# Kernel tuning notes

Measured on AMD Instinct MI355X. Metric: run time of the kernel, lower is better.

## Reference

```python
import jax, jax.numpy as jnp
import numpy as np

F = 1024      # features
CF = 768      # context_features
H = 8         # num_heads
D = 64        # head_features
MID = H * D   # 512
SCALE = D ** -0.5


def _ln(x, g, b):
    m = jnp.mean(x, axis=-1, keepdims=True)
    v = jnp.var(x, axis=-1, keepdims=True)
    return (x - m) / jnp.sqrt(v + 1e-5) * g + b


def _attention(x, ctx, ng, nb, ncg, ncb, wq, wkv, wo, bo):
    # pre-norms (Attention.forward)
    xn = _ln(x, ng, nb)
    cn = _ln(ctx, ncg, ncb)
    q = xn @ wq                              # [b, n, MID]
    k, v = jnp.split(cn @ wkv, 2, axis=-1)   # [b, m, MID] each
    b, n, _ = q.shape
    m = k.shape[1]
    q = q.reshape(b, n, H, D).transpose(0, 2, 1, 3)  # b h n d
    k = k.reshape(b, m, H, D).transpose(0, 2, 1, 3)
    v = v.reshape(b, m, H, D).transpose(0, 2, 1, 3)
    sim = jnp.einsum('bhnd,bhmd->bhnm', q, k) * SCALE   # use_rel_pos=False
    attn = jax.nn.softmax(sim, axis=-1)
    out = jnp.einsum('bhnm,bhmd->bhnd', attn, v)
    out = out.transpose(0, 2, 1, 3).reshape(b, n, MID)
    return out @ wo + bo


def setup_inputs() -> dict:
    key = jax.random.key(0)
    ks = jax.random.split(key, 16)
    s = 0.02
    inp = {
        'x': jax.random.normal(ks[0], (4, 2048, F), jnp.float32),
        'context': jax.random.normal(ks[1], (4, 512, CF), jnp.float32),
        # self-attention params
        'sa_ng': jnp.ones((F,), jnp.float32),
        'sa_nb': jnp.zeros((F,), jnp.float32),
        'sa_ncg': jnp.ones((F,), jnp.float32),
        'sa_ncb': jnp.zeros((F,), jnp.float32),
        'sa_wq': jax.random.normal(ks[2], (F, MID), jnp.float32) * s,
        'sa_wkv': jax.random.normal(ks[3], (F, 2 * MID), jnp.float32) * s,
        'sa_wo': jax.random.normal(ks[4], (MID, F), jnp.float32) * s,
        'sa_bo': jnp.zeros((F,), jnp.float32),
        # cross-attention params
        'ca_ng': jnp.ones((F,), jnp.float32),
        'ca_nb': jnp.zeros((F,), jnp.float32),
        'ca_ncg': jnp.ones((CF,), jnp.float32),
        'ca_ncb': jnp.zeros((CF,), jnp.float32),
        'ca_wq': jax.random.normal(ks[5], (F, MID), jnp.float32) * s,
        'ca_wkv': jax.random.normal(ks[6], (CF, 2 * MID), jnp.float32) * s,
        'ca_wo': jax.random.normal(ks[7], (MID, F), jnp.float32) * s,
        'ca_bo': jnp.zeros((F,), jnp.float32),
    }
    return inp


def reference(x, context,
              sa_ng, sa_nb, sa_ncg, sa_ncb, sa_wq, sa_wkv, sa_wo, sa_bo,
              ca_ng, ca_nb, ca_ncg, ca_ncb, ca_wq, ca_wkv, ca_wo, ca_bo):
    # AttentionBlock.forward: x = self_attn(x) + x; x = cross_attn(x, ctx) + x
    x = _attention(x, x, sa_ng, sa_nb, sa_ncg, sa_ncb, sa_wq, sa_wkv, sa_wo, sa_bo) + x
    x = _attention(x, context, ca_ng, ca_nb, ca_ncg, ca_ncb, ca_wq, ca_wkv, ca_wo, ca_bo) + x
    return x
```

## Files before the change

kernel.cpp:

```cpp
#include <hip/hip_runtime.h>
#include <hip/hip_bf16.h>

typedef __bf16 bf16x8 __attribute__((ext_vector_type(8)));
typedef float  f32x4  __attribute__((ext_vector_type(4)));

#define MFMA16(a, b, c) __builtin_amdgcn_mfma_f32_16x16x32_bf16((a), (b), (c), 0, 0, 0)

__device__ __forceinline__ float fast_exp2(float x) {
#if __has_builtin(__builtin_amdgcn_exp2f)
    return __builtin_amdgcn_exp2f(x);
#else
    return exp2f(x);
#endif
}

__device__ __forceinline__ void async16(void* lds, const void* g) {
    __builtin_amdgcn_global_load_lds(
        (const __attribute__((address_space(1))) unsigned int*)g,
        (__attribute__((address_space(3))) unsigned int*)lds, 16, 0, 0);
}

__device__ __forceinline__ void tconv_tile(const float* __restrict__ W,
                                           __bf16* __restrict__ WT,
                                           int K, int N, int id, int nbx,
                                           __bf16 (*t)[65]) {
    int n0 = (id % nbx) * 64, k0 = (id / nbx) * 64;
    int tx = threadIdx.x & 63, ty = threadIdx.x >> 6;
#pragma unroll
    for (int r = ty; r < 64; r += 4)
        t[r][tx] = (__bf16)W[(size_t)(k0 + r) * N + n0 + tx];
    __syncthreads();
#pragma unroll
    for (int rr = ty; rr < 64; rr += 4)
        WT[(size_t)(n0 + rr) * K + k0 + tx] = t[tx][rr];
}

__global__ __launch_bounds__(256) void tconv6_kernel(
    const float* W0, __bf16* T0, const float* W1, __bf16* T1,
    const float* W2, __bf16* T2, const float* W3, __bf16* T3,
    const float* W4, __bf16* T4, const float* W5, __bf16* T5) {
    __shared__ __bf16 t[64][65];
    int id = blockIdx.x;
    if (id < 128)      tconv_tile(W0, T0, 1024, 512,  id,       8,  t);
    else if (id < 384) tconv_tile(W1, T1, 1024, 1024, id - 128, 16, t);
    else if (id < 512) tconv_tile(W2, T2, 512,  1024, id - 384, 16, t);
    else if (id < 640) tconv_tile(W3, T3, 1024, 512,  id - 512, 8,  t);
    else if (id < 832) tconv_tile(W4, T4, 768,  1024, id - 640, 16, t);
    else               tconv_tile(W5, T5, 512,  1024, id - 832, 16, t);
}

template <int C>
__device__ __forceinline__ void ln_body(const float* __restrict__ xr,
                                        const float* __restrict__ g,
                                        const float* __restrict__ b,
                                        __bf16* __restrict__ orow,
                                        float* p1, float* p2) {
    constexpr int NP = (C == 1024) ? 4 : 3;
    float v[NP], s1 = 0.f, s2 = 0.f;
    if constexpr (C == 1024) {
        float4 f = *(const float4*)&xr[threadIdx.x * 4];
        v[0] = f.x; v[1] = f.y; v[2] = f.z; v[3] = f.w;
#pragma unroll
        for (int i = 0; i < 4; i++) { s1 += v[i]; s2 += v[i] * v[i]; }
    } else {
#pragma unroll
        for (int i = 0; i < 3; i++) {
            v[i] = xr[threadIdx.x + i * 256];
            s1 += v[i]; s2 += v[i] * v[i];
        }
    }
#pragma unroll
    for (int off = 1; off < 64; off <<= 1) {
        s1 += __shfl_xor(s1, off);
        s2 += __shfl_xor(s2, off);
    }
    int wave = threadIdx.x >> 6;
    if ((threadIdx.x & 63) == 0) { p1[wave] = s1; p2[wave] = s2; }
    __syncthreads();
    s1 = p1[0] + p1[1] + p1[2] + p1[3];
    s2 = p2[0] + p2[1] + p2[2] + p2[3];
    float mean = s1 / C;
    float rstd = rsqrtf(s2 / C - mean * mean + 1e-5f);
    if constexpr (C == 1024) {
        union { __bf16 h[4]; unsigned long long u; } pk;
#pragma unroll
        for (int i = 0; i < 4; i++) {
            int c = threadIdx.x * 4 + i;
            pk.h[i] = (__bf16)((v[i] - mean) * rstd * g[c] + b[c]);
        }
        *(unsigned long long*)&orow[threadIdx.x * 4] = pk.u;
    } else {
#pragma unroll
        for (int i = 0; i < 3; i++) {
            int c = threadIdx.x + i * 256;
            orow[c] = (__bf16)((v[i] - mean) * rstd * g[c] + b[c]);
        }
    }
}

__global__ __launch_bounds__(256) void ln2_kernel(const float* __restrict__ x,
                                                  const float* __restrict__ g1,
                                                  const float* __restrict__ b1,
                                                  const float* __restrict__ g2,
                                                  const float* __restrict__ b2,
                                                  __bf16* __restrict__ o1,
                                                  __bf16* __restrict__ o2) {
    constexpr int C = 1024;
    int row = blockIdx.x;
    const float* xr = x + (size_t)row * C;
    float4 f = *(const float4*)&xr[threadIdx.x * 4];
    float v[4] = {f.x, f.y, f.z, f.w};
    float s1 = 0.f, s2 = 0.f;
#pragma unroll
    for (int i = 0; i < 4; i++) { s1 += v[i]; s2 += v[i] * v[i]; }
#pragma unroll
    for (int off = 1; off < 64; off <<= 1) {
        s1 += __shfl_xor(s1, off);
        s2 += __shfl_xor(s2, off);
    }
    __shared__ float p1[4], p2[4];
    int wave = threadIdx.x >> 6;
    if ((threadIdx.x & 63) == 0) { p1[wave] = s1; p2[wave] = s2; }
    __syncthreads();
    s1 = p1[0] + p1[1] + p1[2] + p1[3];
    s2 = p2[0] + p2[1] + p2[2] + p2[3];
    float mean = s1 / C;
    float rstd = rsqrtf(s2 / C - mean * mean + 1e-5f);
    union { __bf16 h[4]; unsigned long long u; } pk1, pk2;
#pragma unroll
    for (int i = 0; i < 4; i++) {
        int c = threadIdx.x * 4 + i;
        float nv = (v[i] - mean) * rstd;
        pk1.h[i] = (__bf16)(nv * g1[c] + b1[c]);
        pk2.h[i] = (__bf16)(nv * g2[c] + b2[c]);
    }
    *(unsigned long long*)&o1[(size_t)row * C + threadIdx.x * 4] = pk1.u;
    *(unsigned long long*)&o2[(size_t)row * C + threadIdx.x * 4] = pk2.u;
}

__global__ __launch_bounds__(256) void ln_cross_kernel(
    const float* __restrict__ x1, const float* __restrict__ g1, const float* __restrict__ b1,
    __bf16* __restrict__ o1,
    const float* __restrict__ ctx, const float* __restrict__ g2, const float* __restrict__ b2,
    __bf16* __restrict__ o2, int rows1) {
    __shared__ float p1[4], p2[4];
    int id = blockIdx.x;
    if (id < rows1) {
        ln_body<1024>(x1 + (size_t)id * 1024, g1, b1, o1 + (size_t)id * 1024, p1, p2);
    } else {
        int row = id - rows1;
        ln_body<768>(ctx + (size_t)row * 768, g2, b2, o2 + (size_t)row * 768, p1, p2);
    }
}

template <int EPI>
__device__ __forceinline__ void gemm_core(const __bf16* __restrict__ A,
                                          const __bf16* __restrict__ BT,
                                          void* __restrict__ Cout,
                                          int N, int K, int bm, int bn,
                                          const float* __restrict__ bias,
                                          const float* __restrict__ res,
                                          float scale,
                                          __bf16* Al, __bf16* Bl) {
    int tid = threadIdx.x;
    int lane = tid & 63, wave = tid >> 6;
    int quad = lane >> 4, l15 = lane & 15;
    int wm = wave >> 1, wn = wave & 1;
    const __bf16* Ab = A + (size_t)(bm * 128) * K;
    const __bf16* Bb = BT + (size_t)(bn * 128) * K;
    f32x4 acc[4][4] = {};
    for (int k0 = 0; k0 < K; k0 += 64) {
#pragma unroll
        for (int j = 0; j < 4; j++) {
            int sbase = wave * 256 + j * 64;
            int s = sbase + lane;
            int r = s >> 3, c = (s & 7) ^ (r & 7);
            async16((char*)Al + sbase * 16, &Ab[(size_t)r * K + k0 + c * 8]);
            async16((char*)Bl + sbase * 16, &Bb[(size_t)r * K + k0 + c * 8]);
        }
        __syncthreads();
#pragma unroll
        for (int ks = 0; ks < 2; ks++) {
            bf16x8 a[4], b[4];
#pragma unroll
            for (int i = 0; i < 4; i++) {
                int row = wm * 64 + i * 16 + l15;
                a[i] = *(const bf16x8*)&Al[row * 64 + ((ks * 4 + quad) ^ (row & 7)) * 8];
            }
#pragma unroll
            for (int t = 0; t < 4; t++) {
                int row = wn * 64 + t * 16 + l15;
                b[t] = *(const bf16x8*)&Bl[row * 64 + ((ks * 4 + quad) ^ (row & 7)) * 8];
            }
#pragma unroll
            for (int i = 0; i < 4; i++)
#pragma unroll
                for (int t = 0; t < 4; t++) acc[i][t] = MFMA16(a[i], b[t], acc[i][t]);
        }
        __syncthreads();
    }
#pragma unroll
    for (int i = 0; i < 4; i++) {
#pragma unroll
        for (int t = 0; t < 4; t++) {
#pragma unroll
            for (int r = 0; r < 4; r++) {
                int row = bm * 128 + wm * 64 + i * 16 + quad * 4 + r;
                int col = bn * 128 + wn * 64 + t * 16 + l15;
                float vv = acc[i][t][r];
                if (EPI == 0) {
                    ((__bf16*)Cout)[(size_t)row * N + col] = (__bf16)(vv * scale);
                } else {
                    ((float*)Cout)[(size_t)row * N + col] =
                        vv + bias[col] + res[(size_t)row * N + col];
                }
            }
        }
    }
}

template <int EPI>
__global__ __launch_bounds__(256) void gemm_bt(const __bf16* __restrict__ A,
                                               const __bf16* __restrict__ BT,
                                               void* __restrict__ Cout,
                                               int M, int N, int K,
                                               const float* __restrict__ bias,
                                               const float* __restrict__ res) {
    __shared__ __align__(16) __bf16 Al[128 * 64];
    __shared__ __align__(16) __bf16 Bl[128 * 64];
    gemm_core<EPI>(A, BT, Cout, N, K, blockIdx.x, blockIdx.y, bias, res, 1.0f, Al, Bl);
}

__global__ __launch_bounds__(256) void gemm_fused3(
    const __bf16* A0, const __bf16* B0, __bf16* C0, int N0, int K0, int nbn0, float sc0,
    const __bf16* A1, const __bf16* B1, __bf16* C1, int N1, int K1, int nbn1, float sc1,
    const __bf16* A2, const __bf16* B2, __bf16* C2, int N2, int K2, int nbn2, float sc2,
    int c0, int c1) {
    __shared__ __align__(16) __bf16 Al[128 * 64];
    __shared__ __align__(16) __bf16 Bl[128 * 64];
    int id = blockIdx.x;
    if (id < c0) {
        gemm_core<0>(A0, B0, C0, N0, K0, id / nbn0, id % nbn0, nullptr, nullptr, sc0, Al, Bl);
    } else if (id < c1) {
        id -= c0;
        gemm_core<0>(A1, B1, C1, N1, K1, id / nbn1, id % nbn1, nullptr, nullptr, sc1, Al, Bl);
    } else {
        id -= c1;
        gemm_core<0>(A2, B2, C2, N2, K2, id / nbn2, id % nbn2, nullptr, nullptr, sc2, Al, Bl);
    }
}

__global__ __launch_bounds__(256) void flash_kernel(const __bf16* __restrict__ q,
                                                    const __bf16* __restrict__ kb,
                                                    const __bf16* __restrict__ vt,
                                                    __bf16* __restrict__ out,
                                                    int n, int m) {
    __shared__ __align__(16) __bf16 Qs[64 * 64];
    __shared__ __align__(16) __bf16 Ks[64 * 64];
    __shared__ __align__(16) __bf16 VTs[64 * 64];
    __shared__ __align__(16) __bf16 Ps[64 * 64];
    int tid = threadIdx.x;
    int lane = tid & 63, w = tid >> 6;
    int quad = lane >> 4, l15 = lane & 15;
    int qt = blockIdx.x, h = blockIdx.y, b = blockIdx.z;
    const size_t BM = (size_t)gridDim.z * m;
    const int qrow = w * 16 + l15;

#pragma unroll
    for (int j = 0; j < 2; j++) {
        int sbase = w * 128 + j * 64;
        int s = sbase + lane;
        int r = s >> 3, c = (s & 7) ^ (r & 7);
        async16((char*)Qs + sbase * 16,
                &q[(size_t)(b * n + qt * 64 + r) * 512 + h * 64 + c * 8]);
    }

    f32x4 acc[4] = {};
    float l_part = 0.f;

    int nkt = m / 64;
    for (int kt = 0; kt < nkt; kt++) {
#pragma unroll
        for (int j = 0; j < 2; j++) {
            int sbase = w * 128 + j * 64;
            int s = sbase + lane;
            int r = s >> 3, c = (s & 7) ^ (r & 7);
            async16((char*)Ks + sbase * 16,
                    &kb[(size_t)(b * m + kt * 64 + r) * 512 + h * 64 + c * 8]);
            async16((char*)VTs + sbase * 16,
                    &vt[(size_t)(h * 64 + r) * BM + b * m + kt * 64 + c * 8]);
        }
        __syncthreads();

        f32x4 sacc[4] = {};
#pragma unroll
        for (int kk = 0; kk < 64; kk += 32) {
            int jb = ((kk >> 3) + quad) ^ (qrow & 7);
            bf16x8 bq = *(const bf16x8*)&Qs[qrow * 64 + jb * 8];
#pragma unroll
            for (int t = 0; t < 4; t++) {
                int krow = t * 16 + l15;
                int ja = ((kk >> 3) + quad) ^ (krow & 7);
                bf16x8 ak = *(const bf16x8*)&Ks[krow * 64 + ja * 8];
                sacc[t] = MFMA16(ak, bq, sacc[t]);
            }
        }

#pragma unroll
        for (int t = 0; t < 4; t++) {
            float e0 = fast_exp2(sacc[t][0]);
            float e1 = fast_exp2(sacc[t][1]);
            float e2 = fast_exp2(sacc[t][2]);
            float e3 = fast_exp2(sacc[t][3]);
            l_part += (e0 + e1) + (e2 + e3);
            union { __bf16 h[4]; unsigned long long u; } pk;
            pk.h[0] = (__bf16)e0; pk.h[1] = (__bf16)e1;
            pk.h[2] = (__bf16)e2; pk.h[3] = (__bf16)e3;
            int chunk = t * 2 + (quad >> 1);
            int off = qrow * 64 + (chunk ^ (qrow & 7)) * 8 + (quad & 1) * 4;
            *(unsigned long long*)&Ps[off] = pk.u;
        }

#pragma unroll
        for (int kk = 0; kk < 64; kk += 32) {
            int jp = ((kk >> 3) + quad) ^ (qrow & 7);
            bf16x8 ap = *(const bf16x8*)&Ps[qrow * 64 + jp * 8];
#pragma unroll
            for (int t2 = 0; t2 < 4; t2++) {
                int drow = t2 * 16 + l15;
                int jv = ((kk >> 3) + quad) ^ (drow & 7);
                bf16x8 bv = *(const bf16x8*)&VTs[drow * 64 + jv * 8];
                acc[t2] = MFMA16(ap, bv, acc[t2]);
            }
        }
        __syncthreads();
    }

    l_part += __shfl_xor(l_part, 16);
    l_part += __shfl_xor(l_part, 32);
    float rinv = 1.0f / l_part;
#pragma unroll
    for (int r = 0; r < 4; r++) {
        float rl = __shfl(rinv, quad * 4 + r);
        int row = b * n + qt * 64 + w * 16 + quad * 4 + r;
#pragma unroll
        for (int t2 = 0; t2 < 4; t2++)
            out[(size_t)row * 512 + h * 64 + t2 * 16 + l15] =
                (__bf16)(acc[t2][r] * rl);
    }
}

extern "C" void kernel_launch(void* const* d_in, const int* in_sizes, int n_in,
                              void* d_out, int out_size, void* d_ws, size_t ws_size,
                              hipStream_t stream) {
    const float* x      = (const float*)d_in[0];
    const float* ctx    = (const float*)d_in[1];
    const float* sa_ng  = (const float*)d_in[2];
    const float* sa_nb  = (const float*)d_in[3];
    const float* sa_ncg = (const float*)d_in[4];
    const float* sa_ncb = (const float*)d_in[5];
    const float* sa_wq  = (const float*)d_in[6];
    const float* sa_wkv = (const float*)d_in[7];
    const float* sa_wo  = (const float*)d_in[8];
    const float* sa_bo  = (const float*)d_in[9];
    const float* ca_ng  = (const float*)d_in[10];
    const float* ca_nb  = (const float*)d_in[11];
    const float* ca_ncg = (const float*)d_in[12];
    const float* ca_ncb = (const float*)d_in[13];
    const float* ca_wq  = (const float*)d_in[14];
    const float* ca_wkv = (const float*)d_in[15];
    const float* ca_wo  = (const float*)d_in[16];
    const float* ca_bo  = (const float*)d_in[17];
    float* out = (float*)d_out;

    const int B = 4, N = 2048, M = 512, F = 1024, CF = 768, MID = 512;
    const int ROWS = B * N;
    const int CROWS = B * M;
    const float QSCALE = 0.125f * 1.4426950408889634f;

    char* ws = (char*)d_ws;
    size_t off = 0;
    auto alloc = [&](size_t bytes) {
        void* p = ws + off;
        off = (off + bytes + 255) & ~(size_t)255;
        return p;
    };
    __bf16* wqT   = (__bf16*)alloc((size_t)MID * F * 2);
    __bf16* wkvT  = (__bf16*)alloc((size_t)(2 * MID) * F * 2);
    __bf16* woT   = (__bf16*)alloc((size_t)F * MID * 2);
    __bf16* cwqT  = (__bf16*)alloc((size_t)MID * F * 2);
    __bf16* cwkvT = (__bf16*)alloc((size_t)(2 * MID) * CF * 2);
    __bf16* cwoT  = (__bf16*)alloc((size_t)F * MID * 2);
    __bf16* xn1   = (__bf16*)alloc((size_t)ROWS * F * 2);
    __bf16* xn2   = (__bf16*)alloc((size_t)ROWS * F * 2);
    __bf16* qb    = (__bf16*)alloc((size_t)ROWS * MID * 2);
    __bf16* kb    = (__bf16*)alloc((size_t)ROWS * MID * 2);
    __bf16* vt    = (__bf16*)alloc((size_t)MID * ROWS * 2);
    __bf16* ao    = (__bf16*)alloc((size_t)ROWS * MID * 2);
    float*  x1    = (float*)alloc((size_t)ROWS * F * 4);
    (void)ws_size; (void)in_sizes; (void)n_in; (void)out_size;

    dim3 blk(256);

    tconv6_kernel<<<dim3(960), blk, 0, stream>>>(
        sa_wq, wqT, sa_wkv, wkvT, sa_wo, woT, ca_wq, cwqT, ca_wkv, cwkvT, ca_wo, cwoT);

    ln2_kernel<<<dim3(ROWS), blk, 0, stream>>>(x, sa_ng, sa_nb, sa_ncg, sa_ncb, xn1, xn2);
    {
        int c0 = (ROWS / 128) * (MID / 128);
        int c1 = c0 + (ROWS / 128) * (MID / 128);
        int c2 = c1 + (MID / 128) * (ROWS / 128);
        gemm_fused3<<<dim3(c2), blk, 0, stream>>>(
            xn1, wqT, qb, MID, F, MID / 128, QSCALE,
            xn2, wkvT, kb, MID, F, MID / 128, 1.0f,
            wkvT + (size_t)MID * F, xn2, vt, ROWS, F, ROWS / 128, 1.0f,
            c0, c1);
    }
    flash_kernel<<<dim3(N / 64, 8, B), blk, 0, stream>>>(qb, kb, vt, ao, N, N);
    gemm_bt<1><<<dim3(ROWS / 128, F / 128), blk, 0, stream>>>(
        ao, woT, x1, ROWS, F, MID, sa_bo, x);

    ln_cross_kernel<<<dim3(ROWS + CROWS), blk, 0, stream>>>(
        x1, ca_ng, ca_nb, xn1, ctx, ca_ncg, ca_ncb, xn2, ROWS);
    {
        int c0 = (ROWS / 128) * (MID / 128);
        int c1 = c0 + (CROWS / 128) * (MID / 128);
        int c2 = c1 + (MID / 128) * (CROWS / 128);
        gemm_fused3<<<dim3(c2), blk, 0, stream>>>(
            xn1, cwqT, qb, MID, F, MID / 128, QSCALE,
            xn2, cwkvT, kb, MID, CF, MID / 128, 1.0f,
            cwkvT + (size_t)MID * CF, xn2, vt, CROWS, CF, CROWS / 128, 1.0f,
            c0, c1);
    }
    flash_kernel<<<dim3(N / 64, 8, B), blk, 0, stream>>>(qb, kb, vt, ao, N, M);
    gemm_bt<1><<<dim3(ROWS / 128, F / 128), blk, 0, stream>>>(
        ao, cwoT, out, ROWS, F, MID, ca_bo, x1);
}
```

Baseline: 314.8 us.

## Rewrite flash attention with 32x32 MFMA and register-resident P

The flash attention kernel now uses 32x32x16 bf16 MFMA tiles instead of 16x16x32, with 128 query rows per block and two waves of 64 rows each. The softmax probabilities are repacked into MFMA operand layout with a cross-half-wave shuffle rather than staged through an LDS buffer, which removes the P shared-memory round trip and one LDS array. Each K/V tile is reused across more query rows. In exchange, blocks have fewer waves, the grid halves, and register pressure from the 16-wide accumulators rises, which may lower occupancy.

```diff
diff --git a/kernel.cpp b/kernel.cpp
--- a/kernel.cpp
+++ b/kernel.cpp
@@ -3,8 +3,10 @@
 
 typedef __bf16 bf16x8 __attribute__((ext_vector_type(8)));
 typedef float  f32x4  __attribute__((ext_vector_type(4)));
+typedef float  f32x16 __attribute__((ext_vector_type(16)));
 
 #define MFMA16(a, b, c) __builtin_amdgcn_mfma_f32_16x16x32_bf16((a), (b), (c), 0, 0, 0)
+#define MFMA32(a, b, c) __builtin_amdgcn_mfma_f32_32x32x16_bf16((a), (b), (c), 0, 0, 0)
 
 __device__ __forceinline__ float fast_exp2(float x) {
 #if __has_builtin(__builtin_amdgcn_exp2f)
@@ -250,39 +252,37 @@
     }
 }
 
-__global__ __launch_bounds__(256) void flash_kernel(const __bf16* __restrict__ q,
+__global__ __launch_bounds__(128) void flash_kernel(const __bf16* __restrict__ q,
                                                     const __bf16* __restrict__ kb,
                                                     const __bf16* __restrict__ vt,
                                                     __bf16* __restrict__ out,
                                                     int n, int m) {
-    __shared__ __align__(16) __bf16 Qs[64 * 64];
+    __shared__ __align__(16) __bf16 Qs[128 * 64];
     __shared__ __align__(16) __bf16 Ks[64 * 64];
     __shared__ __align__(16) __bf16 VTs[64 * 64];
-    __shared__ __align__(16) __bf16 Ps[64 * 64];
     int tid = threadIdx.x;
     int lane = tid & 63, w = tid >> 6;
-    int quad = lane >> 4, l15 = lane & 15;
+    int l31 = lane & 31, l5 = lane >> 5;
     int qt = blockIdx.x, h = blockIdx.y, b = blockIdx.z;
     const size_t BM = (size_t)gridDim.z * m;
-    const int qrow = w * 16 + l15;
-
-#pragma unroll
-    for (int j = 0; j < 2; j++) {
-        int sbase = w * 128 + j * 64;
+
+#pragma unroll
+    for (int j = 0; j < 8; j++) {
+        int sbase = w * 512 + j * 64;
         int s = sbase + lane;
         int r = s >> 3, c = (s & 7) ^ (r & 7);
         async16((char*)Qs + sbase * 16,
-                &q[(size_t)(b * n + qt * 64 + r) * 512 + h * 64 + c * 8]);
-    }
-
-    f32x4 acc[4] = {};
-    float l_part = 0.f;
+                &q[(size_t)(b * n + qt * 128 + r) * 512 + h * 64 + c * 8]);
+    }
+
+    f32x16 acc[2][2] = {};
+    float l_acc[2] = {0.f, 0.f};
 
     int nkt = m / 64;
     for (int kt = 0; kt < nkt; kt++) {
 #pragma unroll
-        for (int j = 0; j < 2; j++) {
-            int sbase = w * 128 + j * 64;
+        for (int j = 0; j < 4; j++) {
+            int sbase = w * 256 + j * 64;
             int s = sbase + lane;
             int r = s >> 3, c = (s & 7) ^ (r & 7);
             async16((char*)Ks + sbase * 16,
@@ -292,61 +292,82 @@
         }
         __syncthreads();
 
-        f32x4 sacc[4] = {};
-#pragma unroll
-        for (int kk = 0; kk < 64; kk += 32) {
-            int jb = ((kk >> 3) + quad) ^ (qrow & 7);
-            bf16x8 bq = *(const bf16x8*)&Qs[qrow * 64 + jb * 8];
-#pragma unroll
-            for (int t = 0; t < 4; t++) {
-                int krow = t * 16 + l15;
-                int ja = ((kk >> 3) + quad) ^ (krow & 7);
-                bf16x8 ak = *(const bf16x8*)&Ks[krow * 64 + ja * 8];
-                sacc[t] = MFMA16(ak, bq, sacc[t]);
-            }
-        }
-
-#pragma unroll
-        for (int t = 0; t < 4; t++) {
-            float e0 = fast_exp2(sacc[t][0]);
-            float e1 = fast_exp2(sacc[t][1]);
-            float e2 = fast_exp2(sacc[t][2]);
-            float e3 = fast_exp2(sacc[t][3]);
-            l_part += (e0 + e1) + (e2 + e3);
-            union { __bf16 h[4]; unsigned long long u; } pk;
-            pk.h[0] = (__bf16)e0; pk.h[1] = (__bf16)e1;
-            pk.h[2] = (__bf16)e2; pk.h[3] = (__bf16)e3;
-            int chunk = t * 2 + (quad >> 1);
-            int off = qrow * 64 + (chunk ^ (qrow & 7)) * 8 + (quad & 1) * 4;
-            *(unsigned long long*)&Ps[off] = pk.u;
-        }
-
-#pragma unroll
-        for (int kk = 0; kk < 64; kk += 32) {
-            int jp = ((kk >> 3) + quad) ^ (qrow & 7);
-            bf16x8 ap = *(const bf16x8*)&Ps[qrow * 64 + jp * 8];
-#pragma unroll
-            for (int t2 = 0; t2 < 4; t2++) {
-                int drow = t2 * 16 + l15;
-                int jv = ((kk >> 3) + quad) ^ (drow & 7);
-                bf16x8 bv = *(const bf16x8*)&VTs[drow * 64 + jv * 8];
-                acc[t2] = MFMA16(ap, bv, acc[t2]);
+#pragma unroll
+        for (int mt = 0; mt < 2; mt++) {
+            f32x16 sacc[2] = {};
+#pragma unroll
+            for (int c = 0; c < 4; c++) {
+                int krow = mt * 32 + l31;
+                bf16x8 ak = *(const bf16x8*)&Ks[krow * 64 + ((2 * c + l5) ^ (krow & 7)) * 8];
+#pragma unroll
+                for (int nt = 0; nt < 2; nt++) {
+                    int qrow = w * 64 + nt * 32 + l31;
+                    bf16x8 bq = *(const bf16x8*)&Qs[qrow * 64 + ((2 * c + l5) ^ (qrow & 7)) * 8];
+                    sacc[nt] = MFMA32(ak, bq, sacc[nt]);
+                }
+            }
+            unsigned long long pk[2][4], sh[2][4];
+#pragma unroll
+            for (int nt = 0; nt < 2; nt++) {
+#pragma unroll
+                for (int s = 0; s < 4; s++) {
+                    float e0 = fast_exp2(sacc[nt][s * 4 + 0]);
+                    float e1 = fast_exp2(sacc[nt][s * 4 + 1]);
+                    float e2 = fast_exp2(sacc[nt][s * 4 + 2]);
+                    float e3 = fast_exp2(sacc[nt][s * 4 + 3]);
+                    l_acc[nt] += (e0 + e1) + (e2 + e3);
+                    union { __bf16 hh[4]; unsigned long long u; } u;
+                    u.hh[0] = (__bf16)e0; u.hh[1] = (__bf16)e1;
+                    u.hh[2] = (__bf16)e2; u.hh[3] = (__bf16)e3;
+                    pk[nt][s] = u.u;
+                }
+#pragma unroll
+                for (int s = 0; s < 4; s++)
+                    sh[nt][s] = __shfl_xor((unsigned long long)pk[nt][s], 32);
+            }
+#pragma unroll
+            for (int c2 = 0; c2 < 2; c2++) {
+#pragma unroll
+                for (int nt = 0; nt < 2; nt++) {
+                    int s0 = 2 * c2, s1 = 2 * c2 + 1;
+                    unsigned long long h0 = (l5 == 0) ? pk[nt][s0] : sh[nt][s1];
+                    unsigned long long h1 = (l5 == 0) ? sh[nt][s0] : pk[nt][s1];
+                    union { unsigned long long u[2]; bf16x8 v; } bu;
+                    bu.u[0] = h0; bu.u[1] = h1;
+#pragma unroll
+                    for (int mtd = 0; mtd < 2; mtd++) {
+                        int drow = mtd * 32 + l31;
+                        int kchunk = 2 * (2 * mt + c2) + l5;
+                        bf16x8 av = *(const bf16x8*)&VTs[drow * 64 + (kchunk ^ (drow & 7)) * 8];
+                        acc[mtd][nt] = MFMA32(av, bu.v, acc[mtd][nt]);
+                    }
+                }
             }
         }
         __syncthreads();
     }
 
-    l_part += __shfl_xor(l_part, 16);
-    l_part += __shfl_xor(l_part, 32);
-    float rinv = 1.0f / l_part;
-#pragma unroll
-    for (int r = 0; r < 4; r++) {
-        float rl = __shfl(rinv, quad * 4 + r);
-        int row = b * n + qt * 64 + w * 16 + quad * 4 + r;
-#pragma unroll
-        for (int t2 = 0; t2 < 4; t2++)
-            out[(size_t)row * 512 + h * 64 + t2 * 16 + l15] =
-                (__bf16)(acc[t2][r] * rl);
+    float linv[2];
+#pragma unroll
+    for (int nt = 0; nt < 2; nt++) {
+        float tot = l_acc[nt] + __shfl_xor(l_acc[nt], 32);
+        linv[nt] = 1.0f / tot;
+    }
+#pragma unroll
+    for (int nt = 0; nt < 2; nt++) {
+        size_t qrow = (size_t)(b * n + qt * 128 + w * 64 + nt * 32 + l31);
+#pragma unroll
+        for (int mtd = 0; mtd < 2; mtd++) {
+#pragma unroll
+            for (int s = 0; s < 4; s++) {
+                union { __bf16 hh[4]; unsigned long long u; } u;
+#pragma unroll
+                for (int r = 0; r < 4; r++)
+                    u.hh[r] = (__bf16)(acc[mtd][nt][s * 4 + r] * linv[nt]);
+                int d = mtd * 32 + s * 8 + l5 * 4;
+                *(unsigned long long*)&out[qrow * 512 + h * 64 + d] = u.u;
+            }
+        }
     }
 }
 
@@ -401,6 +422,7 @@
     (void)ws_size; (void)in_sizes; (void)n_in; (void)out_size;
 
     dim3 blk(256);
+    dim3 fblk(128);
 
     tconv6_kernel<<<dim3(960), blk, 0, stream>>>(
         sa_wq, wqT, sa_wkv, wkvT, sa_wo, woT, ca_wq, cwqT, ca_wkv, cwkvT, ca_wo, cwoT);
@@ -416,7 +438,7 @@
             wkvT + (size_t)MID * F, xn2, vt, ROWS, F, ROWS / 128, 1.0f,
             c0, c1);
     }
-    flash_kernel<<<dim3(N / 64, 8, B), blk, 0, stream>>>(qb, kb, vt, ao, N, N);
+    flash_kernel<<<dim3(N / 128, 8, B), fblk, 0, stream>>>(qb, kb, vt, ao, N, N);
     gemm_bt<1><<<dim3(ROWS / 128, F / 128), blk, 0, stream>>>(
         ao, woT, x1, ROWS, F, MID, sa_bo, x);
 
@@ -432,7 +454,7 @@
             cwkvT + (size_t)MID * CF, xn2, vt, CROWS, CF, CROWS / 128, 1.0f,
             c0, c1);
     }
-    flash_kernel<<<dim3(N / 64, 8, B), blk, 0, stream>>>(qb, kb, vt, ao, N, M);
+    flash_kernel<<<dim3(N / 128, 8, B), fblk, 0, stream>>>(qb, kb, vt, ao, N, M);
     gemm_bt<1><<<dim3(ROWS / 128, F / 128), blk, 0, stream>>>(
         ao, cwoT, out, ROWS, F, MID, ca_bo, x1);
 }
```

Result: slower. 327.0 us (+3.9%).
